# Kernel optimization log

Hardware: AMD Instinct MI355X
Metric: run time of the kernel (lower is better)

Reference implementation:

```python
import jax, jax.numpy as jnp
import numpy as np

N_NODES = 100_000
N_EDGES = 1_600_000
D_FEAT = 32


def setup_inputs() -> dict:
    key = jax.random.key(0)
    k1, k2, k3 = jax.random.split(key, 3)
    features = jax.random.normal(k1, (N_NODES, D_FEAT), dtype=jnp.float32)
    edge_src = jax.random.randint(k2, (N_EDGES,), 0, N_NODES, dtype=jnp.int64)
    edge_dst = jax.random.randint(k3, (N_EDGES,), 0, N_NODES, dtype=jnp.int64)
    return {"features": features, "edge_src": edge_src, "edge_dst": edge_dst}


def reference(features, edge_src, edge_dst):
    # features: [N, D]; edge_src/edge_dst: [E] (neighbor j -> node i), no self-loops.
    N, D = features.shape
    dt = features.dtype
    # deg(i) = |adj_lists[i]| = number of incident (dst) edges
    deg = jax.ops.segment_sum(jnp.ones(edge_dst.shape, dtype=dt), edge_dst, num_segments=N)
    # add self-loops (samp_neighs includes the node itself)
    loop = jnp.arange(N, dtype=edge_src.dtype)
    src = jnp.concatenate([edge_src, loop])
    dst = jnp.concatenate([edge_dst, loop])
    # w_ij = 1 / sqrt((1 + deg(i)) * (1 + deg(j)))
    w = jax.lax.rsqrt((1.0 + deg[dst]) * (1.0 + deg[src]))  # [E+N]
    # to_feats[i] = sum_j w_ij * features[j]
    return jax.ops.segment_sum(w[:, None] * features[src], dst, num_segments=N)
```

## Files before the change

kernel.cpp:

```cpp
#include <hip/hip_runtime.h>

#define D_FEAT 32
#define RSH 8
#define RS_NODES 256
#define LOCAL_SHIFT 24
#define SRC_MASK 0x00FFFFFFu
#define NR_PAD 512
#define BF_CHUNK 3328
#define GATHER_BLOCKS 2048

__device__ __forceinline__ unsigned bfpack(float lo, float hi) {
    unsigned ul = __float_as_uint(lo), uh = __float_as_uint(hi);
    ul = (ul + 0x7FFFu + ((ul >> 16) & 1u)) >> 16;
    uh = (uh + 0x7FFFu + ((uh >> 16) & 1u)) >> 16;
    return ul | (uh << 16);
}

__device__ __forceinline__ void bfadd(float4& a, uint2 w) {
    a.x += __uint_as_float(w.x << 16);
    a.y += __uint_as_float(w.x & 0xFFFF0000u);
    a.z += __uint_as_float(w.y << 16);
    a.w += __uint_as_float(w.y & 0xFFFF0000u);
}

__global__ void binfuse_kernel(const int* __restrict__ src, const int* __restrict__ dst,
                               unsigned* __restrict__ cnt,
                               unsigned* __restrict__ binned,
                               int E, int NR, int CAP) {
    __shared__ unsigned sedge[BF_CHUNK];
    __shared__ unsigned short skey[BF_CHUNK];
    __shared__ unsigned hist[NR_PAD];
    __shared__ unsigned base_l[NR_PAD];
    int lo = blockIdx.x * BF_CHUNK;
    int n = min(BF_CHUNK, E - lo);
    if (n <= 0) return;
    for (int i = threadIdx.x; i < NR; i += blockDim.x) hist[i] = 0u;
    __syncthreads();
    for (int i = threadIdx.x; i < n; i += blockDim.x) {
        int s = src[lo + i];
        int d = dst[lo + i];
        sedge[i] = (unsigned)s | ((unsigned)(d & (RS_NODES - 1)) << LOCAL_SHIFT);
        unsigned r = (unsigned)d >> RSH;
        skey[i] = (unsigned short)r;
        atomicAdd(&hist[r], 1u);
    }
    __syncthreads();
    for (int r = threadIdx.x; r < NR; r += blockDim.x) {
        unsigned c = hist[r];
        base_l[r] = c ? atomicAdd(&cnt[r], c) : 0u;
    }
    __syncthreads();
    for (int i = threadIdx.x; i < NR; i += blockDim.x) hist[i] = 0u;
    __syncthreads();
    for (int i = threadIdx.x; i < n; i += blockDim.x) {
        unsigned r = skey[i];
        unsigned off = base_l[r] + atomicAdd(&hist[r], 1u);
        if (off < (unsigned)CAP)
            binned[(size_t)r * CAP + off] = sedge[i];
    }
}

__global__ void build_kernel(const unsigned* __restrict__ binned, const unsigned* __restrict__ cnt,
                             const float* __restrict__ feat, unsigned* __restrict__ wf,
                             unsigned* __restrict__ csr, uint2* __restrict__ ni,
                             int N, int E, int NR, int CAP) {
    __shared__ unsigned sc[2][NR_PAD];
    __shared__ unsigned deg_l[RS_NODES];
    __shared__ unsigned cur_l[RS_NODES];
    __shared__ float sinv[RS_NODES];
    __shared__ unsigned wtot[4];
    int r = blockIdx.x;
    int tid = threadIdx.x;
    sc[0][tid]       = (tid < NR)       ? min(cnt[tid], (unsigned)CAP)       : 0u;
    sc[0][tid + 256] = (tid + 256 < NR) ? min(cnt[tid + 256], (unsigned)CAP) : 0u;
    int pin = 0;
    for (int off = 1; off < NR_PAD; off <<= 1) {
        __syncthreads();
        int po = pin ^ 1;
        #pragma unroll
        for (int k = 0; k < 2; k++) {
            int idx = tid + k * 256;
            unsigned x = sc[pin][idx];
            if (idx >= off) x += sc[pin][idx - off];
            sc[po][idx] = x;
        }
        pin ^= 1;
    }
    __syncthreads();
    unsigned dense0 = (r == 0) ? 0u : sc[pin][r - 1];
    unsigned cntr = min(cnt[r], (unsigned)CAP);
    size_t seg = (size_t)r * CAP;
    deg_l[tid] = 0u;
    __syncthreads();
    for (unsigned e = tid; e < cntr; e += RS_NODES)
        atomicAdd(&deg_l[binned[seg + e] >> LOCAL_SHIFT], 1u);
    __syncthreads();
    unsigned d = deg_l[tid];
    int lane = tid & 63, w = tid >> 6;
    unsigned incl = d;
    #pragma unroll
    for (int off = 1; off < 64; off <<= 1) {
        unsigned t = __shfl_up(incl, off, 64);
        if (lane >= off) incl += t;
    }
    if (lane == 63) wtot[w] = incl;
    __syncthreads();
    unsigned woff = 0;
    #pragma unroll
    for (int i = 0; i < 4; i++) if (i < w) woff += wtot[i];
    unsigned base = dense0 + woff + incl - d;
    cur_l[tid] = base;
    float ivv = rsqrtf(1.0f + (float)d);
    sinv[tid] = ivv;
    int node = r * RS_NODES + tid;
    if (node < N) ni[node] = make_uint2(base, __float_as_uint(ivv));
    if (r == 0 && tid == 0) ni[N] = make_uint2((unsigned)E, 0u);
    __syncthreads();
    for (unsigned e = tid; e < cntr; e += RS_NODES) {
        unsigned p = binned[seg + e];
        unsigned pos = atomicAdd(&cur_l[p >> LOCAL_SHIFT], 1u);
        csr[pos] = p & SRC_MASK;
    }
    for (int i = tid; i < RS_NODES * 4; i += RS_NODES) {
        int nl = i >> 2, q = i & 3;
        int nn = r * RS_NODES + nl;
        if (nn < N) {
            float iw = sinv[nl];
            const float4* fp = (const float4*)(feat + (size_t)nn * D_FEAT + q * 8);
            float4 a = fp[0], b = fp[1];
            uint4 o;
            o.x = bfpack(iw * a.x, iw * a.y);
            o.y = bfpack(iw * a.z, iw * a.w);
            o.z = bfpack(iw * b.x, iw * b.y);
            o.w = bfpack(iw * b.z, iw * b.w);
            ((uint4*)wf)[(size_t)nn * 4 + q] = o;
        }
    }
}

__global__ void gather_kernel(const unsigned* __restrict__ wf, const unsigned* __restrict__ csr,
                              const uint2* __restrict__ ni, float* __restrict__ out,
                              int N, int per) {
    int w = blockIdx.x * (blockDim.x >> 6) + (threadIdx.x >> 6);
    int lane = threadIdx.x & 63;
    int g = lane >> 3;
    int q = lane & 7;
    int n0 = w * per;
    int n1 = min(N, n0 + per);
    if (n0 >= n1) return;
    uint2 cur = ni[n0];
    for (int node = n0; node < n1; ++node) {
        uint2 nxt = ni[node + 1];
        unsigned start = cur.x, end = nxt.x;
        float iv = __uint_as_float(cur.y);
        float4 acc = make_float4(0.f, 0.f, 0.f, 0.f);
        uint2 ws = *(const uint2*)(wf + (size_t)node * 16 + q * 2);
        if (g == 0) bfadd(acc, ws);
        unsigned k0 = start + g, k1 = start + 8 + g;
        unsigned j0 = (k0 < end) ? csr[k0] : (unsigned)node;
        unsigned j1 = (k1 < end) ? csr[k1] : (unsigned)node;
        uint2 w0 = *(const uint2*)(wf + (size_t)j0 * 16 + q * 2);
        uint2 w1 = *(const uint2*)(wf + (size_t)j1 * 16 + q * 2);
        if (k0 < end) bfadd(acc, w0);
        if (k1 < end) bfadd(acc, w1);
        unsigned k = start + 16 + g;
        if (k < end) {
            for (; k + 8 < end; k += 16) {
                unsigned ja = csr[k], jb = csr[k + 8];
                uint2 wa = *(const uint2*)(wf + (size_t)ja * 16 + q * 2);
                uint2 wb = *(const uint2*)(wf + (size_t)jb * 16 + q * 2);
                bfadd(acc, wa);
                bfadd(acc, wb);
            }
            if (k < end) {
                unsigned jc = csr[k];
                uint2 wc = *(const uint2*)(wf + (size_t)jc * 16 + q * 2);
                bfadd(acc, wc);
            }
        }
        #pragma unroll
        for (int off = 8; off < 64; off <<= 1) {
            acc.x += __shfl_xor(acc.x, off);
            acc.y += __shfl_xor(acc.y, off);
            acc.z += __shfl_xor(acc.z, off);
            acc.w += __shfl_xor(acc.w, off);
        }
        if (g == 0) {
            float4 rv;
            rv.x = iv * acc.x; rv.y = iv * acc.y; rv.z = iv * acc.z; rv.w = iv * acc.w;
            *(float4*)(out + (size_t)node * D_FEAT + q * 4) = rv;
        }
        cur = nxt;
    }
}


__global__ void fb_deg_kernel(const int* __restrict__ dst, float* __restrict__ deg, int E) {
    int i = blockIdx.x * blockDim.x + threadIdx.x;
    int stride = gridDim.x * blockDim.x;
    for (; i < E; i += stride) atomicAdd(&deg[dst[i]], 1.0f);
}
__global__ void fb_inv_kernel(const float* __restrict__ deg, float* __restrict__ inv, int N) {
    int i = blockIdx.x * blockDim.x + threadIdx.x;
    if (i < N) inv[i] = rsqrtf(1.0f + deg[i]);
}
__global__ void fb_scatter_kernel(const float* __restrict__ feat, const int* __restrict__ src,
                                  const int* __restrict__ dst, const float* __restrict__ inv,
                                  float* __restrict__ out, int E) {
    long long tid = (long long)blockIdx.x * blockDim.x + threadIdx.x;
    int e = (int)(tid >> 5);
    int d = (int)(tid & 31);
    if (e >= E) return;
    int s = src[e];
    int t = dst[e];
    atomicAdd(&out[t * D_FEAT + d], inv[s] * feat[s * D_FEAT + d]);
}
__global__ void fb_finalize_kernel(const float* __restrict__ feat, const float* __restrict__ inv,
                                   float* __restrict__ out, int ND) {
    int tid = blockIdx.x * blockDim.x + threadIdx.x;
    if (tid >= ND) return;
    float iv = inv[tid >> 5];
    out[tid] = iv * (out[tid] + iv * feat[tid]);
}

extern "C" void kernel_launch(void* const* d_in, const int* in_sizes, int n_in,
                              void* d_out, int out_size, void* d_ws, size_t ws_size,
                              hipStream_t stream) {
    const float* feat = (const float*)d_in[0];
    const int* esrc = (const int*)d_in[1];
    const int* edst = (const int*)d_in[2];
    float* out = (float*)d_out;

    const int N = in_sizes[0] / D_FEAT;
    const int E = in_sizes[1];
    const int ND = N * D_FEAT;
    const int NR = (N + RS_NODES - 1) >> RSH;

    int CAP = (E + NR - 1) / NR;
    CAP = CAP + CAP / 2 + 256;
    CAP = (CAP + 63) & ~63;

    size_t binned_off = NR;
    size_t csr_off = binned_off + (size_t)NR * CAP;
    size_t wf_off = (csr_off + (size_t)E + 3) & ~(size_t)3;
    size_t ni_off = (wf_off + 16 * (size_t)N + 1) & ~(size_t)1;
    size_t need = (ni_off + 2 * ((size_t)N + 1)) * 4;

    if (ws_size >= need && NR <= NR_PAD && N <= (1 << LOCAL_SHIFT)) {
        unsigned* ws_u   = (unsigned*)d_ws;
        unsigned* cnt    = ws_u;
        unsigned* binned = ws_u + binned_off;
        unsigned* csr    = ws_u + csr_off;
        unsigned* wf     = ws_u + wf_off;
        uint2*    ni     = (uint2*)(ws_u + ni_off);

        hipMemsetAsync(cnt, 0, (size_t)NR * sizeof(unsigned), stream);
        {
            int grid = (E + BF_CHUNK - 1) / BF_CHUNK;
            binfuse_kernel<<<grid, 256, 0, stream>>>(esrc, edst, cnt, binned, E, NR, CAP);
        }
        build_kernel<<<NR, RS_NODES, 0, stream>>>(binned, cnt, feat, wf, csr, ni, N, E, NR, CAP);
        {
            int total_waves = GATHER_BLOCKS * 4;
            int per = (N + total_waves - 1) / total_waves;
            gather_kernel<<<GATHER_BLOCKS, 256, 0, stream>>>(wf, csr, ni, out, N, per);
        }
    } else {
        float* deg = (float*)d_ws;
        float* inv = deg + N;
        hipMemsetAsync(deg, 0, (size_t)N * sizeof(float), stream);
        hipMemsetAsync(out, 0, (size_t)ND * sizeof(float), stream);
        {
            int grid = (E + 255) / 256; if (grid > 2048) grid = 2048;
            fb_deg_kernel<<<grid, 256, 0, stream>>>(edst, deg, E);
        }
        fb_inv_kernel<<<(N + 255) / 256, 256, 0, stream>>>(deg, inv, N);
        {
            long long total = (long long)E * D_FEAT;
            fb_scatter_kernel<<<(int)((total + 255) / 256), 256, 0, stream>>>(feat, esrc, edst, inv, out, E);
        }
        fb_finalize_kernel<<<(ND + 255) / 256, 256, 0, stream>>>(feat, inv, out, ND);
    }
}
```

Baseline: 84.66 us.

## Split bf16 feature table into two halves and gather each in a separate pass

```diff
diff --git a/kernel.cpp b/kernel.cpp
--- a/kernel.cpp
+++ b/kernel.cpp
@@ -61,7 +61,8 @@
 }
 
 __global__ void build_kernel(const unsigned* __restrict__ binned, const unsigned* __restrict__ cnt,
-                             const float* __restrict__ feat, unsigned* __restrict__ wf,
+                             const float* __restrict__ feat,
+                             unsigned* __restrict__ wf_lo, unsigned* __restrict__ wf_hi,
                              unsigned* __restrict__ csr, uint2* __restrict__ ni,
                              int N, int E, int NR, int CAP) {
     __shared__ unsigned sc[2][NR_PAD];
@@ -133,18 +134,19 @@
             o.y = bfpack(iw * a.z, iw * a.w);
             o.z = bfpack(iw * b.x, iw * b.y);
             o.w = bfpack(iw * b.z, iw * b.w);
-            ((uint4*)wf)[(size_t)nn * 4 + q] = o;
-        }
-    }
-}
-
-__global__ void gather_kernel(const unsigned* __restrict__ wf, const unsigned* __restrict__ csr,
-                              const uint2* __restrict__ ni, float* __restrict__ out,
+            unsigned* dest = (q < 2) ? wf_lo : wf_hi;
+            ((uint4*)dest)[(size_t)nn * 2 + (q & 1)] = o;
+        }
+    }
+}
+
+__global__ void gather_kernel(const unsigned* __restrict__ wfh, const unsigned* __restrict__ csr,
+                              const uint2* __restrict__ ni, float* __restrict__ outh,
                               int N, int per) {
     int w = blockIdx.x * (blockDim.x >> 6) + (threadIdx.x >> 6);
     int lane = threadIdx.x & 63;
-    int g = lane >> 3;
-    int q = lane & 7;
+    int g = lane >> 2;
+    int q = lane & 3;
     int n0 = w * per;
     int n1 = min(N, n0 + per);
     if (n0 >= n1) return;
@@ -154,32 +156,23 @@
         unsigned start = cur.x, end = nxt.x;
         float iv = __uint_as_float(cur.y);
         float4 acc = make_float4(0.f, 0.f, 0.f, 0.f);
-        uint2 ws = *(const uint2*)(wf + (size_t)node * 16 + q * 2);
+        uint2 ws = *(const uint2*)(wfh + (size_t)node * 8 + q * 2);
         if (g == 0) bfadd(acc, ws);
-        unsigned k0 = start + g, k1 = start + 8 + g;
+        unsigned k0 = start + g, k1 = start + 16 + g;
         unsigned j0 = (k0 < end) ? csr[k0] : (unsigned)node;
         unsigned j1 = (k1 < end) ? csr[k1] : (unsigned)node;
-        uint2 w0 = *(const uint2*)(wf + (size_t)j0 * 16 + q * 2);
-        uint2 w1 = *(const uint2*)(wf + (size_t)j1 * 16 + q * 2);
+        uint2 w0 = *(const uint2*)(wfh + (size_t)j0 * 8 + q * 2);
+        uint2 w1 = *(const uint2*)(wfh + (size_t)j1 * 8 + q * 2);
         if (k0 < end) bfadd(acc, w0);
         if (k1 < end) bfadd(acc, w1);
-        unsigned k = start + 16 + g;
-        if (k < end) {
-            for (; k + 8 < end; k += 16) {
-                unsigned ja = csr[k], jb = csr[k + 8];
-                uint2 wa = *(const uint2*)(wf + (size_t)ja * 16 + q * 2);
-                uint2 wb = *(const uint2*)(wf + (size_t)jb * 16 + q * 2);
-                bfadd(acc, wa);
-                bfadd(acc, wb);
-            }
-            if (k < end) {
-                unsigned jc = csr[k];
-                uint2 wc = *(const uint2*)(wf + (size_t)jc * 16 + q * 2);
-                bfadd(acc, wc);
-            }
+        unsigned k = start + 32 + g;
+        for (; k < end; k += 16) {
+            unsigned j = csr[k];
+            uint2 wv = *(const uint2*)(wfh + (size_t)j * 8 + q * 2);
+            bfadd(acc, wv);
         }
         #pragma unroll
-        for (int off = 8; off < 64; off <<= 1) {
+        for (int off = 4; off < 64; off <<= 1) {
             acc.x += __shfl_xor(acc.x, off);
             acc.y += __shfl_xor(acc.y, off);
             acc.z += __shfl_xor(acc.z, off);
@@ -188,7 +181,7 @@
         if (g == 0) {
             float4 rv;
             rv.x = iv * acc.x; rv.y = iv * acc.y; rv.z = iv * acc.z; rv.w = iv * acc.w;
-            *(float4*)(out + (size_t)node * D_FEAT + q * 4) = rv;
+            *(float4*)(outh + (size_t)node * D_FEAT + q * 4) = rv;
         }
         cur = nxt;
     }
@@ -242,8 +235,9 @@
 
     size_t binned_off = NR;
     size_t csr_off = binned_off + (size_t)NR * CAP;
-    size_t wf_off = (csr_off + (size_t)E + 3) & ~(size_t)3;
-    size_t ni_off = (wf_off + 16 * (size_t)N + 1) & ~(size_t)1;
+    size_t wflo_off = (csr_off + (size_t)E + 3) & ~(size_t)3;
+    size_t wfhi_off = wflo_off + 8 * (size_t)N;
+    size_t ni_off = (wfhi_off + 8 * (size_t)N + 1) & ~(size_t)1;
     size_t need = (ni_off + 2 * ((size_t)N + 1)) * 4;
 
     if (ws_size >= need && NR <= NR_PAD && N <= (1 << LOCAL_SHIFT)) {
@@ -251,7 +245,8 @@
         unsigned* cnt    = ws_u;
         unsigned* binned = ws_u + binned_off;
         unsigned* csr    = ws_u + csr_off;
-        unsigned* wf     = ws_u + wf_off;
+        unsigned* wf_lo  = ws_u + wflo_off;
+        unsigned* wf_hi  = ws_u + wfhi_off;
         uint2*    ni     = (uint2*)(ws_u + ni_off);
 
         hipMemsetAsync(cnt, 0, (size_t)NR * sizeof(unsigned), stream);
@@ -259,11 +254,12 @@
             int grid = (E + BF_CHUNK - 1) / BF_CHUNK;
             binfuse_kernel<<<grid, 256, 0, stream>>>(esrc, edst, cnt, binned, E, NR, CAP);
         }
-        build_kernel<<<NR, RS_NODES, 0, stream>>>(binned, cnt, feat, wf, csr, ni, N, E, NR, CAP);
+        build_kernel<<<NR, RS_NODES, 0, stream>>>(binned, cnt, feat, wf_lo, wf_hi, csr, ni, N, E, NR, CAP);
         {
             int total_waves = GATHER_BLOCKS * 4;
             int per = (N + total_waves - 1) / total_waves;
-            gather_kernel<<<GATHER_BLOCKS, 256, 0, stream>>>(wf, csr, ni, out, N, per);
+            gather_kernel<<<GATHER_BLOCKS, 256, 0, stream>>>(wf_lo, csr, ni, out, N, per);
+            gather_kernel<<<GATHER_BLOCKS, 256, 0, stream>>>(wf_hi, csr, ni, out + 16, N, per);
         }
     } else {
         float* deg = (float*)d_ws;
```

Result: slower. 104.2 us (+23.1%).
